# Kernel tuning notes

Hardware: AMD Instinct MI355X
Metric: run time of the kernel (lower is better)

Reference implementation:

```python
import jax, jax.numpy as jnp
import numpy as np

N = 50000
IN_CH = 8
HID = 64
OUT_CH = 2
H1 = 4  # heads in gat1
NEG_SLOPE = 0.2
EPS = 1e-16


def setup_inputs() -> dict:
    key = jax.random.key(0)
    ks = jax.random.split(key, 12)
    E = 800000
    x = jax.random.normal(ks[0], (N, IN_CH), dtype=jnp.float32)
    edge_index = jax.random.randint(ks[1], (2, E), 0, N, dtype=jnp.int64)
    # GATConv layer 1: in 8 -> 4 heads x 64, concat -> 256
    s1 = 1.0 / np.sqrt(IN_CH)
    W1 = jax.random.uniform(ks[2], (IN_CH, H1 * HID), jnp.float32, -s1, s1)
    a1_src = jax.random.uniform(ks[3], (H1, HID), jnp.float32, -0.1, 0.1)
    a1_dst = jax.random.uniform(ks[4], (H1, HID), jnp.float32, -0.1, 0.1)
    b1 = jnp.zeros((H1 * HID,), jnp.float32)
    # GATConv layer 2: in 256 -> 1 head x 64
    s2 = 1.0 / np.sqrt(H1 * HID)
    W2 = jax.random.uniform(ks[5], (H1 * HID, HID), jnp.float32, -s2, s2)
    a2_src = jax.random.uniform(ks[6], (1, HID), jnp.float32, -0.1, 0.1)
    a2_dst = jax.random.uniform(ks[7], (1, HID), jnp.float32, -0.1, 0.1)
    b2 = jnp.zeros((HID,), jnp.float32)
    # classifier 64 -> 2
    s3 = 1.0 / np.sqrt(HID)
    Wc = jax.random.uniform(ks[8], (HID, OUT_CH), jnp.float32, -s3, s3)
    bc = jnp.zeros((OUT_CH,), jnp.float32)
    return {
        "x": x, "edge_index": edge_index,
        "W1": W1, "a1_src": a1_src, "a1_dst": a1_dst, "b1": b1,
        "W2": W2, "a2_src": a2_src, "a2_dst": a2_dst, "b2": b2,
        "Wc": Wc, "bc": bc,
    }


def gat_conv(x, src, dst, W, a_src, a_dst, bias, heads, out_ch, concat):
    n = x.shape[0]
    h = (x @ W).reshape(n, heads, out_ch)  # [N,H,C]
    alpha_s = (h * a_src).sum(-1)  # [N,H]
    alpha_d = (h * a_dst).sum(-1)  # [N,H]
    e = alpha_s[src] + alpha_d[dst]  # [E,H]
    e = jnp.where(e > 0, e, NEG_SLOPE * e)  # leaky_relu
    # segment softmax over destination nodes
    m = jax.ops.segment_max(e, dst, num_segments=n)  # [N,H]
    ex = jnp.exp(e - m[dst])
    denom = jax.ops.segment_sum(ex, dst, num_segments=n)  # [N,H]
    alpha = ex / (denom[dst] + EPS)  # [E,H]
    msg = alpha[:, :, None] * h[src]  # [E,H,C]
    out = jax.ops.segment_sum(msg, dst, num_segments=n)  # [N,H,C]
    if concat:
        out = out.reshape(n, heads * out_ch)
    else:
        out = out.mean(axis=1)
    return out + bias


def reference(x, edge_index, W1, a1_src, a1_dst, b1, W2, a2_src, a2_dst, b2, Wc, bc):
    n = x.shape[0]
    loop = jnp.arange(n, dtype=edge_index.dtype)
    src = jnp.concatenate([edge_index[0], loop])
    dst = jnp.concatenate([edge_index[1], loop])
    # dropout p=0.3 is identity in eval mode
    h = gat_conv(x, src, dst, W1, a1_src, a1_dst, b1, H1, HID, concat=True)
    h = jax.nn.elu(h)
    h = gat_conv(h, src, dst, W2, a2_src, a2_dst, b2, 1, HID, concat=True)
    h = jax.nn.elu(h)
    return h @ Wc + bc
```

## Files before the change

kernel.cpp:

```cpp
#include <hip/hip_runtime.h>


__device__ __forceinline__ float lrelu(float e) { return e > 0.f ? e : 0.2f * e; }
__device__ __forceinline__ float eluf(float v)  { return v > 0.f ? v : (__expf(v) - 1.f); }

__device__ __forceinline__ int detect_is64(const int* __restrict__ ei32, int* s_is64) {
    if (threadIdx.x < 64) {
        int w = ei32[2 * threadIdx.x + 1];
        unsigned long long b = __ballot(w != 0);
        if (threadIdx.x == 0) *s_is64 = (b == 0ull) ? 1 : 0;
    }
    __syncthreads();
    return *s_is64;
}

__global__ __launch_bounds__(256) void k1_alpha(
    const float* __restrict__ x, const float* __restrict__ W1,
    const float* __restrict__ a1s, const float* __restrict__ a1d,
    float* __restrict__ aS, float* __restrict__ aD, int* __restrict__ deg, int n) {
    __shared__ float sA1S[32], sA1D[32];
    int t = threadIdx.x;
    if (t < 64) {
        int k = (t & 31) >> 2, h = t & 3;
        const float* av = (t < 32) ? a1s : a1d;
        float ss = 0.f;
        for (int c = 0; c < 64; ++c)
            ss = fmaf(W1[k * 256 + h * 64 + c], av[h * 64 + c], ss);
        if (t < 32) sA1S[t] = ss; else sA1D[t - 32] = ss;
    }
    __syncthreads();
    int node = blockIdx.x * 256 + t;
    if (node >= n) return;
    deg[node] = 0;
    float4 xa = ((const float4*)x)[node * 2];
    float4 xb = ((const float4*)x)[node * 2 + 1];
    float xv[8] = {xa.x, xa.y, xa.z, xa.w, xb.x, xb.y, xb.z, xb.w};
    float s[4], d[4];
#pragma unroll
    for (int h = 0; h < 4; ++h) {
        float ss = 0.f, sd = 0.f;
#pragma unroll
        for (int k = 0; k < 8; ++k) {
            ss = fmaf(xv[k], sA1S[k * 4 + h], ss);
            sd = fmaf(xv[k], sA1D[k * 4 + h], sd);
        }
        s[h] = ss; d[h] = sd;
    }
    ((float4*)aS)[node] = make_float4(s[0], s[1], s[2], s[3]);
    ((float4*)aD)[node] = make_float4(d[0], d[1], d[2], d[3]);
}

__global__ __launch_bounds__(256) void k2_count(
    const int* __restrict__ ei32, int E, int* __restrict__ deg) {
    __shared__ int sf;
    int is64 = detect_is64(ei32, &sf);
    int e = blockIdx.x * 256 + threadIdx.x;
    if (e < E) {
        int d = is64 ? ei32[(E + e) * 2] : ei32[E + e];
        atomicAdd(&deg[d], 1);
    }
}

__global__ __launch_bounds__(1024) void scan_block(
    const int* __restrict__ deg, int n, int* __restrict__ offs, int* __restrict__ bsum) {
    int t = threadIdx.x;
    int i = blockIdx.x * 1024 + t;
    int v = (i < n) ? deg[i] : 0;
    int lane = t & 63, w = t >> 6;
    int s = v;
#pragma unroll
    for (int off = 1; off < 64; off <<= 1) {
        int u = __shfl_up(s, off, 64);
        if (lane >= off) s += u;
    }
    __shared__ int wsums[16];
    if (lane == 63) wsums[w] = s;
    __syncthreads();
    if (t < 16) {
        int wv = wsums[t];
#pragma unroll
        for (int off = 1; off < 16; off <<= 1) {
            int u = __shfl_up(wv, off, 64);
            if (t >= off) wv += u;
        }
        wsums[t] = wv;
    }
    __syncthreads();
    int waveoff = (w == 0) ? 0 : wsums[w - 1];
    if (i < n) offs[i] = s + waveoff - v;
    if (t == 1023) bsum[blockIdx.x] = s + waveoff;
}

__global__ void scan_small(int* __restrict__ bsum, int nb) {
    int t = threadIdx.x;
    int v = (t < nb) ? bsum[t] : 0;
#pragma unroll
    for (int off = 1; off < 64; off <<= 1) {
        int u = __shfl_up(v, off, 64);
        if (t >= off) v += u;
    }
    if (t < nb) bsum[t] = v;
}

__global__ void scan_add(int* __restrict__ offs, const int* __restrict__ bsum,
                         int* __restrict__ cur, int n, int nb) {
    int i = blockIdx.x * blockDim.x + threadIdx.x;
    if (i < n) {
        int b = i >> 10;
        int val = offs[i] + (b ? bsum[b - 1] : 0);
        offs[i] = val;
        cur[i] = val;
    }
    if (i == 0) offs[n] = bsum[nb - 1];
}

__global__ __launch_bounds__(256) void k4_scatter(
    const int* __restrict__ ei32, int E, int* __restrict__ cur,
    int* __restrict__ ssrc) {
    __shared__ int sf;
    int is64 = detect_is64(ei32, &sf);
    int e = blockIdx.x * 256 + threadIdx.x;
    if (e < E) {
        int d = is64 ? ei32[(E + e) * 2] : ei32[E + e];
        int s = is64 ? ei32[e * 2] : ei32[e];
        int p = atomicAdd(&cur[d], 1);
        ssrc[p] = s;
    }
}

__global__ __launch_bounds__(256) void k5_agg1(
    const float* __restrict__ x, const float* __restrict__ aS,
    const float* __restrict__ aD, const int* __restrict__ offs,
    const int* __restrict__ ssrc, const float* __restrict__ W1,
    const float* __restrict__ b1, float* __restrict__ hout, int n) {
    int node = blockIdx.x * 4 + (threadIdx.x >> 6);
    if (node >= n) return;
    int lane = threadIdx.x & 63;
    int h = lane & 3, eslot = lane >> 2;
    int s0 = offs[node], s1 = offs[node + 1];
    float ad = aD[node * 4 + h];
    float denom = 0.f;
    float vec[8] = {0.f, 0.f, 0.f, 0.f, 0.f, 0.f, 0.f, 0.f};
    const float4* xv = (const float4*)x;
    for (int e = s0 + eslot; e < s1; e += 16) {
        int s = ssrc[e];
        float ex = __expf(lrelu(aS[s * 4 + h] + ad));
        denom += ex;
        float4 xa = xv[s * 2];
        float4 xb = xv[s * 2 + 1];
        vec[0] = fmaf(ex, xa.x, vec[0]); vec[1] = fmaf(ex, xa.y, vec[1]);
        vec[2] = fmaf(ex, xa.z, vec[2]); vec[3] = fmaf(ex, xa.w, vec[3]);
        vec[4] = fmaf(ex, xb.x, vec[4]); vec[5] = fmaf(ex, xb.y, vec[5]);
        vec[6] = fmaf(ex, xb.z, vec[6]); vec[7] = fmaf(ex, xb.w, vec[7]);
    }
#pragma unroll
    for (int off = 4; off < 64; off <<= 1) {
        denom += __shfl_xor(denom, off, 64);
#pragma unroll
        for (int k = 0; k < 8; ++k) vec[k] += __shfl_xor(vec[k], off, 64);
    }
    float exs = __expf(lrelu(aS[node * 4 + h] + ad));
    denom += exs;
    float4 xa = xv[node * 2];
    float4 xb = xv[node * 2 + 1];
    vec[0] = fmaf(exs, xa.x, vec[0]); vec[1] = fmaf(exs, xa.y, vec[1]);
    vec[2] = fmaf(exs, xa.z, vec[2]); vec[3] = fmaf(exs, xa.w, vec[3]);
    vec[4] = fmaf(exs, xb.x, vec[4]); vec[5] = fmaf(exs, xb.y, vec[5]);
    vec[6] = fmaf(exs, xb.z, vec[6]); vec[7] = fmaf(exs, xb.w, vec[7]);
    float vhk[4][8], invd[4];
#pragma unroll
    for (int hh = 0; hh < 4; ++hh) {
        invd[hh] = 1.f / (__shfl(denom, hh, 64) + 1e-16f);
#pragma unroll
        for (int k = 0; k < 8; ++k) vhk[hh][k] = __shfl(vec[k], hh, 64);
    }
#pragma unroll
    for (int hh = 0; hh < 4; ++hh) {
        int j = hh * 64 + lane;
        float dot = 0.f;
#pragma unroll
        for (int k = 0; k < 8; ++k) dot = fmaf(vhk[hh][k], W1[k * 256 + j], dot);
        hout[(size_t)node * 256 + j] = eluf(fmaf(dot, invd[hh], b1[j]));
    }
}

__global__ __launch_bounds__(256) void k6_gemm(
    const float* __restrict__ hin, const float* __restrict__ W2,
    const float* __restrict__ a2s, const float* __restrict__ a2d,
    float* __restrict__ h2, float* __restrict__ A2S, float* __restrict__ A2D,
    int n) {
    __shared__ float W2s[128 * 64];
    __shared__ float hs[32 * 256];
    int tid = threadIdx.x;
    int nb0 = blockIdx.x * 32;
    for (int i = tid; i < 2048; i += 256) {
        int row = i >> 6;
        int node = nb0 + row;
        float4 val = make_float4(0.f, 0.f, 0.f, 0.f);
        if (node < n) val = ((const float4*)hin)[(size_t)node * 64 + (i & 63)];
        ((float4*)hs)[i] = val;
    }
    int j = tid & 63, ng = tid >> 6;
    float acc[8];
#pragma unroll
    for (int i = 0; i < 8; ++i) acc[i] = 0.f;
    for (int kc = 0; kc < 2; ++kc) {
        __syncthreads();
        for (int i = tid; i < 2048; i += 256)
            ((float4*)W2s)[i] = ((const float4*)W2)[kc * 2048 + i];
        __syncthreads();
#pragma unroll 4
        for (int k = 0; k < 128; ++k) {
            float w = W2s[k * 64 + j];
#pragma unroll
            for (int i = 0; i < 8; ++i)
                acc[i] = fmaf(hs[(ng * 8 + i) * 256 + kc * 128 + k], w, acc[i]);
        }
    }
    float as_ = a2s[j], ad_ = a2d[j];
#pragma unroll
    for (int i = 0; i < 8; ++i) {
        int node = nb0 + ng * 8 + i;
        if (node < n) h2[(size_t)node * 64 + j] = acc[i];
        float ps = acc[i] * as_, pd = acc[i] * ad_;
#pragma unroll
        for (int off = 32; off > 0; off >>= 1) {
            ps += __shfl_down(ps, off, 64);
            pd += __shfl_down(pd, off, 64);
        }
        if (j == 0 && node < n) { A2S[node] = ps; A2D[node] = pd; }
    }
}

__global__ __launch_bounds__(256) void k7_agg2(
    const float* __restrict__ h2, const float* __restrict__ A2S,
    const float* __restrict__ A2D, const int* __restrict__ offs,
    const int* __restrict__ ssrc, const float* __restrict__ b2,
    const float* __restrict__ Wc, const float* __restrict__ bc,
    float* __restrict__ out, int n) {
    int node = blockIdx.x * 4 + (threadIdx.x >> 6);
    if (node >= n) return;
    int c = threadIdx.x & 63;
    int s0 = offs[node], s1 = offs[node + 1];
    float ad = A2D[node];
    int g = c >> 4, q = c & 15;
    const float4* h2v = (const float4*)h2;
    float denom = 0.f;
    float4 acc = make_float4(0.f, 0.f, 0.f, 0.f);
    for (int e = s0 + g; e < s1; e += 4) {
        int s = ssrc[e];
        float4 hv = h2v[(size_t)s * 16 + q];
        float ex = __expf(lrelu(A2S[s] + ad));
        denom += ex;
        acc.x = fmaf(ex, hv.x, acc.x); acc.y = fmaf(ex, hv.y, acc.y);
        acc.z = fmaf(ex, hv.z, acc.z); acc.w = fmaf(ex, hv.w, acc.w);
    }
#pragma unroll
    for (int off = 16; off <= 32; off <<= 1) {
        denom += __shfl_xor(denom, off, 64);
        acc.x += __shfl_xor(acc.x, off, 64);
        acc.y += __shfl_xor(acc.y, off, 64);
        acc.z += __shfl_xor(acc.z, off, 64);
        acc.w += __shfl_xor(acc.w, off, 64);
    }
    float exs = __expf(lrelu(A2S[node] + ad));
    denom += exs;
    float4 hS = h2v[(size_t)node * 16 + q];
    acc.x = fmaf(exs, hS.x, acc.x); acc.y = fmaf(exs, hS.y, acc.y);
    acc.z = fmaf(exs, hS.z, acc.z); acc.w = fmaf(exs, hS.w, acc.w);
    float inv = 1.f / (denom + 1e-16f);
    float4 bv = ((const float4*)b2)[q];
    float o0 = eluf(fmaf(acc.x, inv, bv.x));
    float o1 = eluf(fmaf(acc.y, inv, bv.y));
    float o2 = eluf(fmaf(acc.z, inv, bv.z));
    float o3 = eluf(fmaf(acc.w, inv, bv.w));
    int ch = q * 4;
    float p0 = o0 * Wc[ch * 2 + 0] + o1 * Wc[ch * 2 + 2] + o2 * Wc[ch * 2 + 4] + o3 * Wc[ch * 2 + 6];
    float p1 = o0 * Wc[ch * 2 + 1] + o1 * Wc[ch * 2 + 3] + o2 * Wc[ch * 2 + 5] + o3 * Wc[ch * 2 + 7];
#pragma unroll
    for (int off = 8; off > 0; off >>= 1) {
        p0 += __shfl_xor(p0, off, 64);
        p1 += __shfl_xor(p1, off, 64);
    }
    if (c == 0) {
        out[(size_t)node * 2 + 0] = p0 + bc[0];
        out[(size_t)node * 2 + 1] = p1 + bc[1];
    }
}

extern "C" void kernel_launch(void* const* d_in, const int* in_sizes, int n_in,
                              void* d_out, int out_size, void* d_ws, size_t ws_size,
                              hipStream_t stream) {
    const float* x   = (const float*)d_in[0];
    const int*   ei  = (const int*)d_in[1];
    const float* W1  = (const float*)d_in[2];
    const float* a1s = (const float*)d_in[3];
    const float* a1d = (const float*)d_in[4];
    const float* b1  = (const float*)d_in[5];
    const float* W2  = (const float*)d_in[6];
    const float* a2s = (const float*)d_in[7];
    const float* a2d = (const float*)d_in[8];
    const float* b2  = (const float*)d_in[9];
    const float* Wc  = (const float*)d_in[10];
    const float* bc  = (const float*)d_in[11];
    float* out = (float*)d_out;
    (void)n_in; (void)out_size; (void)ws_size;

    int n = in_sizes[0] / 8;
    int E = in_sizes[1] / 2;

    char* ws = (char*)d_ws;
    size_t o = 0;
    auto carve = [&](size_t bytes) -> char* {
        char* p = ws + o;
        o = (o + bytes + 255) & ~(size_t)255;
        return p;
    };
    float* hout = (float*)carve((size_t)n * 256 * 4);
    float* h2   = (float*)carve((size_t)n * 64 * 4);
    float* aS   = (float*)carve((size_t)n * 4 * 4);
    float* aD   = (float*)carve((size_t)n * 4 * 4);
    int*   deg  = (int*)carve((size_t)n * 4);
    int*   offs = (int*)carve((size_t)(n + 1) * 4);
    int*   cur  = (int*)carve((size_t)n * 4);
    int*   ssrc = (int*)carve((size_t)E * 4);
    int*   bsum = (int*)carve(64 * 4);
    float* A2S  = (float*)carve((size_t)n * 4);
    float* A2D  = (float*)carve((size_t)n * 4);

    k1_alpha<<<(n + 255) / 256, 256, 0, stream>>>(x, W1, a1s, a1d, aS, aD, deg, n);
    k2_count<<<(E + 255) / 256, 256, 0, stream>>>(ei, E, deg);
    int nb = (n + 1023) / 1024;
    scan_block<<<nb, 1024, 0, stream>>>(deg, n, offs, bsum);
    scan_small<<<1, 64, 0, stream>>>(bsum, nb);
    scan_add<<<(n + 255) / 256, 256, 0, stream>>>(offs, bsum, cur, n, nb);
    k4_scatter<<<(E + 255) / 256, 256, 0, stream>>>(ei, E, cur, ssrc);
    k5_agg1<<<(n + 3) / 4, 256, 0, stream>>>(x, aS, aD, offs, ssrc, W1, b1, hout, n);
    k6_gemm<<<(n + 31) / 32, 256, 0, stream>>>(hout, W2, a2s, a2d, h2, A2S, A2D, n);
    k7_agg2<<<(n + 3) / 4, 256, 0, stream>>>(h2, A2S, A2D, offs, ssrc, b2, Wc, bc, out, n);
}
```

Baseline: 322.1 us.

## Replace FP32 layer-2 GEMM with split-bf16 MFMA using prepacked weight fragments

The scalar FP32 shared-memory GEMM for the second GAT layer is replaced by an MFMA kernel using bf16x8 16x16x32 instructions. To keep roughly FP32 accuracy, both activations and W2 are split into hi/lo bf16 parts and three MFMA products are accumulated per tile. W2 is pre-packed into per-lane fragment order by a new small kernel, and the aggregation kernel now writes two bf16 planes instead of one fp32 buffer. Accuracy drops slightly because the lo*lo term is omitted and the hi/lo split adds conversion work, but the memory traffic stays the same.

```diff
diff --git a/kernel.cpp b/kernel.cpp
--- a/kernel.cpp
+++ b/kernel.cpp
@@ -1,8 +1,20 @@
 #include <hip/hip_runtime.h>
-
+#include <hip/hip_bf16.h>
+
+
+typedef __attribute__((ext_vector_type(8))) short bf16x8;
+typedef __attribute__((ext_vector_type(4))) float f32x4;
 
 __device__ __forceinline__ float lrelu(float e) { return e > 0.f ? e : 0.2f * e; }
 __device__ __forceinline__ float eluf(float v)  { return v > 0.f ? v : (__expf(v) - 1.f); }
+
+__device__ __forceinline__ void split_bf16(float v, unsigned short& hi, unsigned short& lo) {
+    __hip_bfloat16 h = __float2bfloat16(v);
+    float hf = __bfloat162float(h);
+    __hip_bfloat16 l = __float2bfloat16(v - hf);
+    hi = *reinterpret_cast<unsigned short*>(&h);
+    lo = *reinterpret_cast<unsigned short*>(&l);
+}
 
 __device__ __forceinline__ int detect_is64(const int* __restrict__ ei32, int* s_is64) {
     if (threadIdx.x < 64) {
@@ -50,6 +62,28 @@
     ((float4*)aD)[node] = make_float4(d[0], d[1], d[2], d[3]);
 }
 
+__global__ __launch_bounds__(256) void kB_pack(
+    const float* __restrict__ W2, uint4* __restrict__ Bpk) {
+    int idx = blockIdx.x * 256 + threadIdx.x;
+    int lane = idx & 63, rest = idx >> 6;
+    int nt = rest & 3, ks = (rest >> 2) & 7, split = rest >> 5;
+    unsigned short vals[8];
+#pragma unroll
+    for (int i = 0; i < 8; ++i) {
+        int k = ks * 32 + (lane >> 4) * 8 + i;
+        int col = nt * 16 + (lane & 15);
+        unsigned short hi, lo;
+        split_bf16(W2[k * 64 + col], hi, lo);
+        vals[i] = split ? lo : hi;
+    }
+    uint4 w;
+    w.x = (unsigned)vals[0] | ((unsigned)vals[1] << 16);
+    w.y = (unsigned)vals[2] | ((unsigned)vals[3] << 16);
+    w.z = (unsigned)vals[4] | ((unsigned)vals[5] << 16);
+    w.w = (unsigned)vals[6] | ((unsigned)vals[7] << 16);
+    Bpk[rest * 64 + lane] = w;
+}
+
 __global__ __launch_bounds__(256) void k2_count(
     const int* __restrict__ ei32, int E, int* __restrict__ deg) {
     __shared__ int sf;
@@ -132,7 +166,8 @@
     const float* __restrict__ x, const float* __restrict__ aS,
     const float* __restrict__ aD, const int* __restrict__ offs,
     const int* __restrict__ ssrc, const float* __restrict__ W1,
-    const float* __restrict__ b1, float* __restrict__ hout, int n) {
+    const float* __restrict__ b1, unsigned short* __restrict__ hhi,
+    unsigned short* __restrict__ hlo, int n) {
     int node = blockIdx.x * 4 + (threadIdx.x >> 6);
     if (node >= n) return;
     int lane = threadIdx.x & 63;
@@ -180,55 +215,71 @@
         float dot = 0.f;
 #pragma unroll
         for (int k = 0; k < 8; ++k) dot = fmaf(vhk[hh][k], W1[k * 256 + j], dot);
-        hout[(size_t)node * 256 + j] = eluf(fmaf(dot, invd[hh], b1[j]));
-    }
-}
-
-__global__ __launch_bounds__(256) void k6_gemm(
-    const float* __restrict__ hin, const float* __restrict__ W2,
-    const float* __restrict__ a2s, const float* __restrict__ a2d,
-    float* __restrict__ h2, float* __restrict__ A2S, float* __restrict__ A2D,
-    int n) {
-    __shared__ float W2s[128 * 64];
-    __shared__ float hs[32 * 256];
-    int tid = threadIdx.x;
-    int nb0 = blockIdx.x * 32;
-    for (int i = tid; i < 2048; i += 256) {
-        int row = i >> 6;
-        int node = nb0 + row;
-        float4 val = make_float4(0.f, 0.f, 0.f, 0.f);
-        if (node < n) val = ((const float4*)hin)[(size_t)node * 64 + (i & 63)];
-        ((float4*)hs)[i] = val;
-    }
-    int j = tid & 63, ng = tid >> 6;
-    float acc[8];
-#pragma unroll
-    for (int i = 0; i < 8; ++i) acc[i] = 0.f;
-    for (int kc = 0; kc < 2; ++kc) {
-        __syncthreads();
-        for (int i = tid; i < 2048; i += 256)
-            ((float4*)W2s)[i] = ((const float4*)W2)[kc * 2048 + i];
-        __syncthreads();
-#pragma unroll 4
-        for (int k = 0; k < 128; ++k) {
-            float w = W2s[k * 64 + j];
-#pragma unroll
-            for (int i = 0; i < 8; ++i)
-                acc[i] = fmaf(hs[(ng * 8 + i) * 256 + kc * 128 + k], w, acc[i]);
-        }
-    }
-    float as_ = a2s[j], ad_ = a2d[j];
-#pragma unroll
-    for (int i = 0; i < 8; ++i) {
-        int node = nb0 + ng * 8 + i;
-        if (node < n) h2[(size_t)node * 64 + j] = acc[i];
-        float ps = acc[i] * as_, pd = acc[i] * ad_;
-#pragma unroll
-        for (int off = 32; off > 0; off >>= 1) {
-            ps += __shfl_down(ps, off, 64);
-            pd += __shfl_down(pd, off, 64);
-        }
-        if (j == 0 && node < n) { A2S[node] = ps; A2D[node] = pd; }
+        float o = eluf(fmaf(dot, invd[hh], b1[j]));
+        unsigned short hi, lo;
+        split_bf16(o, hi, lo);
+        hhi[(size_t)node * 256 + j] = hi;
+        hlo[(size_t)node * 256 + j] = lo;
+    }
+}
+
+__global__ __launch_bounds__(256) void k6_mfma(
+    const unsigned short* __restrict__ hhi, const unsigned short* __restrict__ hlo,
+    const uint4* __restrict__ Bpk, const float* __restrict__ a2s,
+    const float* __restrict__ a2d, float* __restrict__ h2,
+    float* __restrict__ A2S, float* __restrict__ A2D, int n) {
+    int lane = threadIdx.x & 63;
+    int row0 = blockIdx.x * 64 + (threadIdx.x >> 6) * 16;
+    int r = row0 + (lane & 15);
+    if (r >= n) r = n - 1;
+    f32x4 acc[4];
+#pragma unroll
+    for (int nt = 0; nt < 4; ++nt) acc[nt] = {0.f, 0.f, 0.f, 0.f};
+#pragma unroll
+    for (int ks = 0; ks < 8; ++ks) {
+        int koff = ks * 32 + (lane >> 4) * 8;
+        bf16x8 ahi = *(const bf16x8*)(hhi + (size_t)r * 256 + koff);
+        bf16x8 alo = *(const bf16x8*)(hlo + (size_t)r * 256 + koff);
+#pragma unroll
+        for (int nt = 0; nt < 4; ++nt) {
+            uint4 bh = Bpk[(ks * 4 + nt) * 64 + lane];
+            uint4 bl = Bpk[((8 + ks) * 4 + nt) * 64 + lane];
+            bf16x8 bhi = *(bf16x8*)&bh;
+            bf16x8 blo = *(bf16x8*)&bl;
+            acc[nt] = __builtin_amdgcn_mfma_f32_16x16x32_bf16(ahi, bhi, acc[nt], 0, 0, 0);
+            acc[nt] = __builtin_amdgcn_mfma_f32_16x16x32_bf16(ahi, blo, acc[nt], 0, 0, 0);
+            acc[nt] = __builtin_amdgcn_mfma_f32_16x16x32_bf16(alo, bhi, acc[nt], 0, 0, 0);
+        }
+    }
+#pragma unroll
+    for (int nt = 0; nt < 4; ++nt) {
+#pragma unroll
+        for (int reg = 0; reg < 4; ++reg) {
+            int row = row0 + (lane >> 4) * 4 + reg;
+            if (row < n) h2[(size_t)row * 64 + nt * 16 + (lane & 15)] = acc[nt][reg];
+        }
+    }
+    float a2sv[4], a2dv[4];
+#pragma unroll
+    for (int nt = 0; nt < 4; ++nt) {
+        a2sv[nt] = a2s[nt * 16 + (lane & 15)];
+        a2dv[nt] = a2d[nt * 16 + (lane & 15)];
+    }
+#pragma unroll
+    for (int reg = 0; reg < 4; ++reg) {
+        float ps = 0.f, pd = 0.f;
+#pragma unroll
+        for (int nt = 0; nt < 4; ++nt) {
+            ps = fmaf(acc[nt][reg], a2sv[nt], ps);
+            pd = fmaf(acc[nt][reg], a2dv[nt], pd);
+        }
+#pragma unroll
+        for (int off = 1; off < 16; off <<= 1) {
+            ps += __shfl_xor(ps, off, 64);
+            pd += __shfl_xor(pd, off, 64);
+        }
+        int row = row0 + (lane >> 4) * 4 + reg;
+        if ((lane & 15) == 0 && row < n) { A2S[row] = ps; A2D[row] = pd; }
     }
 }
 
@@ -316,7 +367,8 @@
         o = (o + bytes + 255) & ~(size_t)255;
         return p;
     };
-    float* hout = (float*)carve((size_t)n * 256 * 4);
+    unsigned short* hhi = (unsigned short*)carve((size_t)n * 256 * 2);
+    unsigned short* hlo = (unsigned short*)carve((size_t)n * 256 * 2);
     float* h2   = (float*)carve((size_t)n * 64 * 4);
     float* aS   = (float*)carve((size_t)n * 4 * 4);
     float* aD   = (float*)carve((size_t)n * 4 * 4);
@@ -325,17 +377,19 @@
     int*   cur  = (int*)carve((size_t)n * 4);
     int*   ssrc = (int*)carve((size_t)E * 4);
     int*   bsum = (int*)carve(64 * 4);
+    uint4* Bpk  = (uint4*)carve(4096 * 16);
     float* A2S  = (float*)carve((size_t)n * 4);
     float* A2D  = (float*)carve((size_t)n * 4);
 
     k1_alpha<<<(n + 255) / 256, 256, 0, stream>>>(x, W1, a1s, a1d, aS, aD, deg, n);
+    kB_pack<<<16, 256, 0, stream>>>(W2, Bpk);
     k2_count<<<(E + 255) / 256, 256, 0, stream>>>(ei, E, deg);
     int nb = (n + 1023) / 1024;
     scan_block<<<nb, 1024, 0, stream>>>(deg, n, offs, bsum);
     scan_small<<<1, 64, 0, stream>>>(bsum, nb);
     scan_add<<<(n + 255) / 256, 256, 0, stream>>>(offs, bsum, cur, n, nb);
     k4_scatter<<<(E + 255) / 256, 256, 0, stream>>>(ei, E, cur, ssrc);
-    k5_agg1<<<(n + 3) / 4, 256, 0, stream>>>(x, aS, aD, offs, ssrc, W1, b1, hout, n);
-    k6_gemm<<<(n + 31) / 32, 256, 0, stream>>>(hout, W2, a2s, a2d, h2, A2S, A2D, n);
+    k5_agg1<<<(n + 3) / 4, 256, 0, stream>>>(x, aS, aD, offs, ssrc, W1, b1, hhi, hlo, n);
+    k6_mfma<<<(n + 63) / 64, 256, 0, stream>>>(hhi, hlo, Bpk, a2s, a2d, h2, A2S, A2D, n);
     k7_agg2<<<(n + 3) / 4, 256, 0, stream>>>(h2, A2S, A2D, offs, ssrc, b2, Wc, bc, out, n);
 }
```

Result: faster. 275.7 us (-14.4%).
